# Kernel optimization log

Measured on AMD Instinct MI355X. Metric: run time of the kernel, lower is better.

Reference implementation:

```python
import jax, jax.numpy as jnp
import numpy as np

NEG_INF = -9e15  # matches the torch source's large-negative mask value
LRELU_SLOPE = 0.2


def setup_inputs() -> dict:
    key = jax.random.key(0)
    k1, k2, k3, k4, k5, k6 = jax.random.split(key, 6)
    N, D_IN, D_OUT = 8192, 512, 256
    h = jax.random.normal(k1, (N, D_IN), dtype=jnp.float32)
    adj = jax.random.randint(k2, (N, N), 0, 2, dtype=jnp.int32)
    # xavier_uniform with gain=1.414 for W [out, in] and a [1, 2*out]
    lim_W = 1.414 * np.sqrt(6.0 / (D_IN + D_OUT))
    lim_a = 1.414 * np.sqrt(6.0 / (2 * D_OUT + 1))
    W_w = jax.random.uniform(k3, (D_OUT, D_IN), minval=-lim_W, maxval=lim_W, dtype=jnp.float32)
    W_b = jax.random.normal(k4, (D_OUT,), dtype=jnp.float32) * 0.01
    a_w = jax.random.uniform(k5, (1, 2 * D_OUT), minval=-lim_a, maxval=lim_a, dtype=jnp.float32)
    a_b = jax.random.normal(k6, (1,), dtype=jnp.float32) * 0.01
    return {"h": h, "adj": adj, "W_w": W_w, "W_b": W_b, "a_w": a_w, "a_b": a_b}


def reference(h, adj, W_w, W_b, a_w, a_b):
    # wh = W(h): [N, d_out]
    wh = h @ W_w.T + W_b
    d_out = wh.shape[-1]
    # a(cat([wh_i, wh_j])) decomposes: a_src . wh_i + a_dst . wh_j + a_b
    # (identical math to the O(N^2 * 2d) repeat/cat in the torch source)
    a_src, a_dst = a_w[0, :d_out], a_w[0, d_out:]
    s_src = wh @ a_src  # [N]
    s_dst = wh @ a_dst  # [N]
    e = jax.nn.leaky_relu(s_src[:, None] + s_dst[None, :] + a_b[0], LRELU_SLOPE)  # [N, N]
    masked = jnp.where(adj > 0, e, jnp.float32(NEG_INF))
    attn = jax.nn.softmax(masked, axis=1)  # softmax over neighbors j
    return attn @ wh  # [N, d_out]
```

## Files before the change

kernel.cpp:

```cpp
#include <hip/hip_runtime.h>

typedef unsigned short ushort_t;
typedef unsigned int uint_t;
typedef __attribute__((ext_vector_type(8))) short short8;
typedef __attribute__((ext_vector_type(4))) float f32x4;
typedef __attribute__((ext_vector_type(4))) int i32x4;
typedef __attribute__((ext_vector_type(4))) uint_t u32x4;
typedef __attribute__((ext_vector_type(4))) ushort_t u16x4;

#define LRELU_SLOPE 0.2f

static __device__ __forceinline__ float bf2f(ushort_t h) {
    uint_t u = ((uint_t)h) << 16;
    return __builtin_bit_cast(float, u);
}
static __device__ __forceinline__ ushort_t f2bf(float f) {
    uint_t u = __builtin_bit_cast(uint_t, f);
    uint_t r = (u + 0x7fffu + ((u >> 16) & 1u)) >> 16;
    return (ushort_t)r;
}

static __device__ __forceinline__ void split4(float4 x, uint2& hi, uint2& lo) {
    ushort_t h0 = f2bf(x.x), h1 = f2bf(x.y), h2 = f2bf(x.z), h3 = f2bf(x.w);
    hi.x = (uint_t)h0 | ((uint_t)h1 << 16);
    hi.y = (uint_t)h2 | ((uint_t)h3 << 16);
    float r0 = x.x - bf2f(h0), r1 = x.y - bf2f(h1);
    float r2 = x.z - bf2f(h2), r3 = x.w - bf2f(h3);
    lo.x = (uint_t)f2bf(r0) | ((uint_t)f2bf(r1) << 16);
    lo.y = (uint_t)f2bf(r2) | ((uint_t)f2bf(r3) << 16);
}

__launch_bounds__(256, 2)
__global__ void k1_gemm(const float* __restrict__ h, const float* __restrict__ W,
                        const float* __restrict__ Wb, const float* __restrict__ aw,
                        ushort_t* __restrict__ whT, float* __restrict__ s_src,
                        float* __restrict__ s_dst) {
    __shared__ __align__(16) ushort_t aHi[256 * 40], aLo[256 * 40];
    __shared__ __align__(16) ushort_t bHi[32 * 40], bLo[32 * 40];
    __shared__ float redLds[2][4][32];

    const int t = threadIdx.x;
    const int wv = t >> 6, ln = t & 63;
    const int i0 = blockIdx.x * 32;
    const int srow = t >> 3, sch = t & 7;

    f32x4 acc[4][2];
#pragma unroll
    for (int mt = 0; mt < 4; ++mt)
#pragma unroll
        for (int nt = 0; nt < 2; ++nt) acc[mt][nt] = (f32x4){0.f, 0.f, 0.f, 0.f};

    for (int k0 = 0; k0 < 512; k0 += 32) {
        __syncthreads();
#pragma unroll
        for (int r = 0; r < 8; ++r) {
            float4 x = *(const float4*)(W + (size_t)(r * 32 + srow) * 512 + k0 + sch * 4);
            uint2 hi, lo;
            split4(x, hi, lo);
            *(uint2*)(aHi + (r * 32 + srow) * 40 + sch * 4) = hi;
            *(uint2*)(aLo + (r * 32 + srow) * 40 + sch * 4) = lo;
        }
        {
            float4 x = *(const float4*)(h + (size_t)(i0 + srow) * 512 + k0 + sch * 4);
            uint2 hi, lo;
            split4(x, hi, lo);
            *(uint2*)(bHi + srow * 40 + sch * 4) = hi;
            *(uint2*)(bLo + srow * 40 + sch * 4) = lo;
        }
        __syncthreads();
        {
            short8 bh[2], bl[2];
#pragma unroll
            for (int nt = 0; nt < 2; ++nt) {
                const int boff = (nt * 16 + (ln & 15)) * 40 + (ln >> 4) * 8;
                bh[nt] = *(const short8*)(bHi + boff);
                bl[nt] = *(const short8*)(bLo + boff);
            }
#pragma unroll
            for (int mt = 0; mt < 4; ++mt) {
                const int aoff = (wv * 64 + mt * 16 + (ln & 15)) * 40 + (ln >> 4) * 8;
                short8 ah = *(const short8*)(aHi + aoff);
                short8 al = *(const short8*)(aLo + aoff);
#pragma unroll
                for (int nt = 0; nt < 2; ++nt) {
                    acc[mt][nt] = __builtin_amdgcn_mfma_f32_16x16x32_bf16(ah, bh[nt], acc[mt][nt], 0, 0, 0);
                    acc[mt][nt] = __builtin_amdgcn_mfma_f32_16x16x32_bf16(ah, bl[nt], acc[mt][nt], 0, 0, 0);
                    acc[mt][nt] = __builtin_amdgcn_mfma_f32_16x16x32_bf16(al, bh[nt], acc[mt][nt], 0, 0, 0);
                }
            }
        }
    }

    float psrc[2] = {0.f, 0.f}, pdst[2] = {0.f, 0.f};
#pragma unroll
    for (int mt = 0; mt < 4; ++mt) {
#pragma unroll
        for (int r = 0; r < 4; ++r) {
            const int o = wv * 64 + mt * 16 + (ln >> 4) * 4 + r;
            const float wbv = Wb[o];
            const float as = aw[o];
            const float ad = aw[256 + o];
#pragma unroll
            for (int nt = 0; nt < 2; ++nt) {
                const float v = acc[mt][nt][r] + wbv;
                psrc[nt] += v * as;
                pdst[nt] += v * ad;
                const int i = i0 + nt * 16 + (ln & 15);
                whT[(size_t)o * 8192 + i] = f2bf(v);
            }
        }
    }
#pragma unroll
    for (int off = 16; off < 64; off <<= 1) {
#pragma unroll
        for (int nt = 0; nt < 2; ++nt) {
            psrc[nt] += __shfl_xor(psrc[nt], off, 64);
            pdst[nt] += __shfl_xor(pdst[nt], off, 64);
        }
    }
    if (ln < 16) {
#pragma unroll
        for (int nt = 0; nt < 2; ++nt) {
            redLds[0][wv][nt * 16 + ln] = psrc[nt];
            redLds[1][wv][nt * 16 + ln] = pdst[nt];
        }
    }
    __syncthreads();
    if (t < 32) {
        float s = 0.f;
#pragma unroll
        for (int w = 0; w < 4; ++w) s += redLds[0][w][t];
        s_src[i0 + t] = s;
    } else if (t < 64) {
        float s = 0.f;
#pragma unroll
        for (int w = 0; w < 4; ++w) s += redLds[1][w][t - 32];
        s_dst[i0 + t - 32] = s;
    }
}

__launch_bounds__(512, 2)
__global__ void k2_attn(const int* __restrict__ adj, const ushort_t* __restrict__ whT,
                        const float* __restrict__ s_src, const float* __restrict__ s_dst,
                        const float* __restrict__ ab_p, float* __restrict__ out) {
    __shared__ __align__(16) ushort_t wLds[256 * 72];
    __shared__ __align__(16) ushort_t pLds[32 * 72];
    __shared__ float zLds[32];

    const int t = threadIdx.x;
    const int wv = t >> 6, ln = t & 63;
    const int dq = wv & 3, kh = wv >> 2;
    const int i0 = blockIdx.x * 32;
    const int prow = t >> 4, pjc = t & 15;
    const int srow = t >> 3, sch = t & 7;

    const float ab = ab_p[0];
    const float ssrc = s_src[i0 + prow];

    const int* aBase = adj + (size_t)(i0 + prow) * 8192 + pjc * 4;
    const float* sBase = s_dst + pjc * 4;
    const ushort_t* wBase = whT + (size_t)srow * 8192 + sch * 8;
    ushort_t* pDst = pLds + prow * 72 + pjc * 4;

    f32x4 acc[2][4];
#pragma unroll
    for (int mt = 0; mt < 2; ++mt)
#pragma unroll
        for (int nt = 0; nt < 4; ++nt) acc[mt][nt] = (f32x4){0.f, 0.f, 0.f, 0.f};
    float zacc = 0.f;

    i32x4 Av = *(const i32x4*)aBase;
    f32x4 Sv = *(const f32x4*)sBase;
    u32x4 Wv[4];
#pragma unroll
    for (int r = 0; r < 4; ++r) Wv[r] = *(const u32x4*)(wBase + (size_t)r * 64 * 8192);

    for (int it = 0; it < 128; ++it) {
        const int jn = (it < 127) ? (it + 1) * 64 : it * 64;
        i32x4 Ac = Av;
        f32x4 Sc = Sv;
        u32x4 Wc[4];
#pragma unroll
        for (int r = 0; r < 4; ++r) Wc[r] = Wv[r];
        Av = *(const i32x4*)(aBase + jn);
        Sv = *(const f32x4*)(sBase + jn);
#pragma unroll
        for (int r = 0; r < 4; ++r) Wv[r] = *(const u32x4*)(wBase + (size_t)r * 64 * 8192 + jn);

        __syncthreads();
#pragma unroll
        for (int r = 0; r < 4; ++r)
            *(u32x4*)(wLds + (r * 64 + srow) * 72 + sch * 8) = Wc[r];
        {
            u16x4 pv4;
            float z4 = 0.f;
#pragma unroll
            for (int k = 0; k < 4; ++k) {
                float sc = ssrc + Sc[k] + ab;
                sc = sc > 0.f ? sc : LRELU_SLOPE * sc;
                sc = fminf(sc, 60.f);
                float pv = (Ac[k] > 0) ? __expf(sc) : 0.f;
                z4 += pv;
                pv4[k] = f2bf(pv);
            }
            zacc += z4;
            *(u16x4*)pDst = pv4;
        }
        __syncthreads();
        {
            short8 b[4];
#pragma unroll
            for (int nt = 0; nt < 4; ++nt)
                b[nt] = *(const short8*)(wLds + (dq * 64 + nt * 16 + (ln & 15)) * 72 + kh * 32 + (ln >> 4) * 8);
#pragma unroll
            for (int mt = 0; mt < 2; ++mt) {
                short8 a = *(const short8*)(pLds + (mt * 16 + (ln & 15)) * 72 + kh * 32 + (ln >> 4) * 8);
#pragma unroll
                for (int nt = 0; nt < 4; ++nt)
                    acc[mt][nt] = __builtin_amdgcn_mfma_f32_16x16x32_bf16(a, b[nt], acc[mt][nt], 0, 0, 0);
            }
        }
    }

    zacc += __shfl_xor(zacc, 1, 64);
    zacc += __shfl_xor(zacc, 2, 64);
    zacc += __shfl_xor(zacc, 4, 64);
    zacc += __shfl_xor(zacc, 8, 64);
    if ((t & 15) == 0) zLds[prow] = 1.0f / fmaxf(zacc, 1e-30f);

    __syncthreads();
    float* ex = (float*)wLds;
    if (kh == 1) {
        float* p = ex + (dq * 64 + ln) * 33;
#pragma unroll
        for (int mt = 0; mt < 2; ++mt)
#pragma unroll
            for (int nt = 0; nt < 4; ++nt)
#pragma unroll
                for (int r = 0; r < 4; ++r) p[mt * 16 + nt * 4 + r] = acc[mt][nt][r];
    }
    __syncthreads();
    if (kh == 0) {
        const float* p = ex + (dq * 64 + ln) * 33;
#pragma unroll
        for (int mt = 0; mt < 2; ++mt)
#pragma unroll
            for (int nt = 0; nt < 4; ++nt)
#pragma unroll
                for (int r = 0; r < 4; ++r) {
                    const int il = mt * 16 + (ln >> 4) * 4 + r;
                    const int d = dq * 64 + nt * 16 + (ln & 15);
                    out[(size_t)(i0 + il) * 256 + d] =
                        (acc[mt][nt][r] + p[mt * 16 + nt * 4 + r]) * zLds[il];
                }
    }
}

extern "C" void kernel_launch(void* const* d_in, const int* in_sizes, int n_in, void* d_out,
                              int out_size, void* d_ws, size_t ws_size, hipStream_t stream) {
    int order[16];
    for (int i = 0; i < n_in; ++i) order[i] = i;
    for (int a = 0; a < n_in; ++a)
        for (int b = a + 1; b < n_in; ++b)
            if (in_sizes[order[b]] < in_sizes[order[a]]) {
                int tmp = order[a]; order[a] = order[b]; order[b] = tmp;
            }
    const float* ab = (const float*)d_in[order[0]];
    const float* Wb = (const float*)d_in[order[1]];
    const float* aw = (const float*)d_in[order[2]];
    const float* Ww = (const float*)d_in[order[3]];
    const float* h = (const float*)d_in[order[4]];
    const int* adj = (const int*)d_in[order[5]];

    char* ws = (char*)d_ws;
    ushort_t* whT = (ushort_t*)ws;
    float* ssrc = (float*)(ws + 4194304);
    float* sdst = (float*)(ws + 4194304 + 32768);

    hipLaunchKernelGGL(k1_gemm, dim3(256), dim3(256), 0, stream, h, Ww, Wb, aw, whT, ssrc, sdst);
    hipLaunchKernelGGL(k2_attn, dim3(256), dim3(512), 0, stream, adj, whT, ssrc, sdst, ab,
                       (float*)d_out);
}
```

Baseline: 485.2 us.

## Load MFMA operands directly from global into registers, drop LDS staging and barriers

Each wave now computes its own probability fragments from adj and s_dst and loads whT fragments straight from global memory in MFMA operand layout, so the per-iteration LDS writes, reads and both __syncthreads are removed. This duplicates exp computation and adj/s_dst loads across the four dq waves, and the whT loads become narrower, more scattered accesses. Launch bounds drop to one block per CU to give room for the extra registers, which lowers occupancy.

```diff
diff --git a/kernel.cpp b/kernel.cpp
--- a/kernel.cpp
+++ b/kernel.cpp
@@ -6,7 +6,6 @@
 typedef __attribute__((ext_vector_type(4))) float f32x4;
 typedef __attribute__((ext_vector_type(4))) int i32x4;
 typedef __attribute__((ext_vector_type(4))) uint_t u32x4;
-typedef __attribute__((ext_vector_type(4))) ushort_t u16x4;
 
 #define LRELU_SLOPE 0.2f
 
@@ -139,97 +138,97 @@
     }
 }
 
-__launch_bounds__(512, 2)
+__launch_bounds__(512, 1)
 __global__ void k2_attn(const int* __restrict__ adj, const ushort_t* __restrict__ whT,
                         const float* __restrict__ s_src, const float* __restrict__ s_dst,
                         const float* __restrict__ ab_p, float* __restrict__ out) {
-    __shared__ __align__(16) ushort_t wLds[256 * 72];
-    __shared__ __align__(16) ushort_t pLds[32 * 72];
-    __shared__ float zLds[32];
+    __shared__ float ex[256 * 33];
+    __shared__ float zA[32], zB[32];
 
     const int t = threadIdx.x;
     const int wv = t >> 6, ln = t & 63;
     const int dq = wv & 3, kh = wv >> 2;
     const int i0 = blockIdx.x * 32;
-    const int prow = t >> 4, pjc = t & 15;
-    const int srow = t >> 3, sch = t & 7;
+    const int row0 = ln & 15, kq = ln >> 4;
 
     const float ab = ab_p[0];
-    const float ssrc = s_src[i0 + prow];
-
-    const int* aBase = adj + (size_t)(i0 + prow) * 8192 + pjc * 4;
-    const float* sBase = s_dst + pjc * 4;
-    const ushort_t* wBase = whT + (size_t)srow * 8192 + sch * 8;
-    ushort_t* pDst = pLds + prow * 72 + pjc * 4;
+    const float sb0 = s_src[i0 + row0] + ab;
+    const float sb1 = s_src[i0 + 16 + row0] + ab;
+
+    const int joff = kh * 32 + kq * 8;
+    const int* aBase0 = adj + (size_t)(i0 + row0) * 8192 + joff;
+    const int* aBase1 = adj + (size_t)(i0 + 16 + row0) * 8192 + joff;
+    const float* sBase = s_dst + joff;
+    const ushort_t* wBase = whT + (size_t)(dq * 64 + row0) * 8192 + joff;
 
     f32x4 acc[2][4];
 #pragma unroll
     for (int mt = 0; mt < 2; ++mt)
 #pragma unroll
         for (int nt = 0; nt < 4; ++nt) acc[mt][nt] = (f32x4){0.f, 0.f, 0.f, 0.f};
-    float zacc = 0.f;
-
-    i32x4 Av = *(const i32x4*)aBase;
-    f32x4 Sv = *(const f32x4*)sBase;
-    u32x4 Wv[4];
-#pragma unroll
-    for (int r = 0; r < 4; ++r) Wv[r] = *(const u32x4*)(wBase + (size_t)r * 64 * 8192);
+    float z0 = 0.f, z1 = 0.f;
+
+    i32x4 A0a = *(const i32x4*)aBase0, A0b = *(const i32x4*)(aBase0 + 4);
+    i32x4 A1a = *(const i32x4*)aBase1, A1b = *(const i32x4*)(aBase1 + 4);
+    f32x4 Sa = *(const f32x4*)sBase, Sb = *(const f32x4*)(sBase + 4);
+    short8 Bf[4];
+#pragma unroll
+    for (int nt = 0; nt < 4; ++nt)
+        Bf[nt] = *(const short8*)(wBase + (size_t)nt * 16 * 8192);
 
     for (int it = 0; it < 128; ++it) {
         const int jn = (it < 127) ? (it + 1) * 64 : it * 64;
-        i32x4 Ac = Av;
-        f32x4 Sc = Sv;
-        u32x4 Wc[4];
-#pragma unroll
-        for (int r = 0; r < 4; ++r) Wc[r] = Wv[r];
-        Av = *(const i32x4*)(aBase + jn);
-        Sv = *(const f32x4*)(sBase + jn);
-#pragma unroll
-        for (int r = 0; r < 4; ++r) Wv[r] = *(const u32x4*)(wBase + (size_t)r * 64 * 8192 + jn);
-
-        __syncthreads();
-#pragma unroll
-        for (int r = 0; r < 4; ++r)
-            *(u32x4*)(wLds + (r * 64 + srow) * 72 + sch * 8) = Wc[r];
-        {
-            u16x4 pv4;
-            float z4 = 0.f;
-#pragma unroll
-            for (int k = 0; k < 4; ++k) {
-                float sc = ssrc + Sc[k] + ab;
-                sc = sc > 0.f ? sc : LRELU_SLOPE * sc;
-                sc = fminf(sc, 60.f);
-                float pv = (Ac[k] > 0) ? __expf(sc) : 0.f;
-                z4 += pv;
-                pv4[k] = f2bf(pv);
-            }
-            zacc += z4;
-            *(u16x4*)pDst = pv4;
-        }
-        __syncthreads();
-        {
-            short8 b[4];
-#pragma unroll
-            for (int nt = 0; nt < 4; ++nt)
-                b[nt] = *(const short8*)(wLds + (dq * 64 + nt * 16 + (ln & 15)) * 72 + kh * 32 + (ln >> 4) * 8);
-#pragma unroll
-            for (int mt = 0; mt < 2; ++mt) {
-                short8 a = *(const short8*)(pLds + (mt * 16 + (ln & 15)) * 72 + kh * 32 + (ln >> 4) * 8);
-#pragma unroll
-                for (int nt = 0; nt < 4; ++nt)
-                    acc[mt][nt] = __builtin_amdgcn_mfma_f32_16x16x32_bf16(a, b[nt], acc[mt][nt], 0, 0, 0);
-            }
-        }
-    }
-
-    zacc += __shfl_xor(zacc, 1, 64);
-    zacc += __shfl_xor(zacc, 2, 64);
-    zacc += __shfl_xor(zacc, 4, 64);
-    zacc += __shfl_xor(zacc, 8, 64);
-    if ((t & 15) == 0) zLds[prow] = 1.0f / fmaxf(zacc, 1e-30f);
-
-    __syncthreads();
-    float* ex = (float*)wLds;
+        i32x4 cA0a = A0a, cA0b = A0b, cA1a = A1a, cA1b = A1b;
+        f32x4 cSa = Sa, cSb = Sb;
+        short8 cB[4];
+#pragma unroll
+        for (int nt = 0; nt < 4; ++nt) cB[nt] = Bf[nt];
+        A0a = *(const i32x4*)(aBase0 + jn);
+        A0b = *(const i32x4*)(aBase0 + jn + 4);
+        A1a = *(const i32x4*)(aBase1 + jn);
+        A1b = *(const i32x4*)(aBase1 + jn + 4);
+        Sa = *(const f32x4*)(sBase + jn);
+        Sb = *(const f32x4*)(sBase + jn + 4);
+#pragma unroll
+        for (int nt = 0; nt < 4; ++nt)
+            Bf[nt] = *(const short8*)(wBase + (size_t)nt * 16 * 8192 + jn);
+
+        short8 af0, af1;
+#pragma unroll
+        for (int e = 0; e < 8; ++e) {
+            const float sd = (e < 4) ? cSa[e] : cSb[e - 4];
+            const int a0 = (e < 4) ? cA0a[e] : cA0b[e - 4];
+            const int a1 = (e < 4) ? cA1a[e] : cA1b[e - 4];
+            float t0 = sb0 + sd;
+            float t1 = sb1 + sd;
+            t0 = fminf(fmaxf(t0, LRELU_SLOPE * t0), 60.f);
+            t1 = fminf(fmaxf(t1, LRELU_SLOPE * t1), 60.f);
+            float p0 = (a0 > 0) ? __expf(t0) : 0.f;
+            float p1 = (a1 > 0) ? __expf(t1) : 0.f;
+            z0 += p0;
+            z1 += p1;
+            af0[e] = (short)f2bf(p0);
+            af1[e] = (short)f2bf(p1);
+        }
+#pragma unroll
+        for (int nt = 0; nt < 4; ++nt) {
+            acc[0][nt] = __builtin_amdgcn_mfma_f32_16x16x32_bf16(af0, cB[nt], acc[0][nt], 0, 0, 0);
+            acc[1][nt] = __builtin_amdgcn_mfma_f32_16x16x32_bf16(af1, cB[nt], acc[1][nt], 0, 0, 0);
+        }
+    }
+
+    z0 += __shfl_xor(z0, 16, 64);
+    z0 += __shfl_xor(z0, 32, 64);
+    z1 += __shfl_xor(z1, 16, 64);
+    z1 += __shfl_xor(z1, 32, 64);
+    if (wv == 0 && ln < 16) {
+        zA[row0] = z0;
+        zA[16 + row0] = z1;
+    }
+    if (wv == 4 && ln < 16) {
+        zB[row0] = z0;
+        zB[16 + row0] = z1;
+    }
     if (kh == 1) {
         float* p = ex + (dq * 64 + ln) * 33;
 #pragma unroll
@@ -245,14 +244,16 @@
 #pragma unroll
         for (int mt = 0; mt < 2; ++mt)
 #pragma unroll
-            for (int nt = 0; nt < 4; ++nt)
-#pragma unroll
-                for (int r = 0; r < 4; ++r) {
-                    const int il = mt * 16 + (ln >> 4) * 4 + r;
-                    const int d = dq * 64 + nt * 16 + (ln & 15);
+            for (int r = 0; r < 4; ++r) {
+                const int il = mt * 16 + kq * 4 + r;
+                const float zinv = 1.0f / fmaxf(zA[il] + zB[il], 1e-30f);
+#pragma unroll
+                for (int nt = 0; nt < 4; ++nt) {
+                    const int d = dq * 64 + nt * 16 + row0;
                     out[(size_t)(i0 + il) * 256 + d] =
-                        (acc[mt][nt][r] + p[mt * 16 + nt * 4 + r]) * zLds[il];
+                        (acc[mt][nt][r] + p[mt * 16 + nt * 4 + r]) * zinv;
                 }
+            }
     }
 }
 
```

Result: slower. 609.6 us (+25.6%).

## Split attention over neighbor halves and drop split-bf16 precision in projection GEMM

Applied to the files above, without the earlier changes.

The projection GEMM now casts W and h straight to bf16, replacing the hi/lo split that needed three MFMAs per tile, and uses a 64-wide K step with the LDS laid out to match. The attention kernel can split the neighbor dimension in two, doubling the grid to 512 blocks, which suits a GPU with more CUs than the old 256 blocks could fill. Each half writes partial sums and softmax denominators, and a new normalization kernel combines them. Occupancy hints are raised. In exchange, wh loses precision, and the split path adds an extra kernel launch and an extra read and write of the output-sized buffer.

```diff
diff --git a/kernel.cpp b/kernel.cpp
--- a/kernel.cpp
+++ b/kernel.cpp
@@ -19,15 +19,13 @@
     uint_t r = (u + 0x7fffu + ((u >> 16) & 1u)) >> 16;
     return (ushort_t)r;
 }
-
-static __device__ __forceinline__ void split4(float4 x, uint2& hi, uint2& lo) {
-    ushort_t h0 = f2bf(x.x), h1 = f2bf(x.y), h2 = f2bf(x.z), h3 = f2bf(x.w);
-    hi.x = (uint_t)h0 | ((uint_t)h1 << 16);
-    hi.y = (uint_t)h2 | ((uint_t)h3 << 16);
-    float r0 = x.x - bf2f(h0), r1 = x.y - bf2f(h1);
-    float r2 = x.z - bf2f(h2), r3 = x.w - bf2f(h3);
-    lo.x = (uint_t)f2bf(r0) | ((uint_t)f2bf(r1) << 16);
-    lo.y = (uint_t)f2bf(r2) | ((uint_t)f2bf(r3) << 16);
+static __device__ __forceinline__ uint4 pack8(float4 a, float4 b) {
+    uint4 r;
+    r.x = (uint_t)f2bf(a.x) | ((uint_t)f2bf(a.y) << 16);
+    r.y = (uint_t)f2bf(a.z) | ((uint_t)f2bf(a.w) << 16);
+    r.z = (uint_t)f2bf(b.x) | ((uint_t)f2bf(b.y) << 16);
+    r.w = (uint_t)f2bf(b.z) | ((uint_t)f2bf(b.w) << 16);
+    return r;
 }
 
 __launch_bounds__(256, 2)
@@ -35,14 +33,15 @@
                         const float* __restrict__ Wb, const float* __restrict__ aw,
                         ushort_t* __restrict__ whT, float* __restrict__ s_src,
                         float* __restrict__ s_dst) {
-    __shared__ __align__(16) ushort_t aHi[256 * 40], aLo[256 * 40];
-    __shared__ __align__(16) ushort_t bHi[32 * 40], bLo[32 * 40];
+    __shared__ __align__(16) ushort_t aT[256 * 72];
+    __shared__ __align__(16) ushort_t bT[32 * 72];
     __shared__ float redLds[2][4][32];
 
     const int t = threadIdx.x;
     const int wv = t >> 6, ln = t & 63;
     const int i0 = blockIdx.x * 32;
     const int srow = t >> 3, sch = t & 7;
+    const int row0 = ln & 15, kq = ln >> 4;
 
     f32x4 acc[4][2];
 #pragma unroll
@@ -50,43 +49,34 @@
 #pragma unroll
         for (int nt = 0; nt < 2; ++nt) acc[mt][nt] = (f32x4){0.f, 0.f, 0.f, 0.f};
 
-    for (int k0 = 0; k0 < 512; k0 += 32) {
+    for (int k0 = 0; k0 < 512; k0 += 64) {
         __syncthreads();
 #pragma unroll
         for (int r = 0; r < 8; ++r) {
-            float4 x = *(const float4*)(W + (size_t)(r * 32 + srow) * 512 + k0 + sch * 4);
-            uint2 hi, lo;
-            split4(x, hi, lo);
-            *(uint2*)(aHi + (r * 32 + srow) * 40 + sch * 4) = hi;
-            *(uint2*)(aLo + (r * 32 + srow) * 40 + sch * 4) = lo;
+            const float* gp = W + (size_t)(r * 32 + srow) * 512 + k0 + sch * 8;
+            float4 x0 = *(const float4*)gp;
+            float4 x1 = *(const float4*)(gp + 4);
+            *(uint4*)(aT + (r * 32 + srow) * 72 + sch * 8) = pack8(x0, x1);
         }
         {
-            float4 x = *(const float4*)(h + (size_t)(i0 + srow) * 512 + k0 + sch * 4);
-            uint2 hi, lo;
-            split4(x, hi, lo);
-            *(uint2*)(bHi + srow * 40 + sch * 4) = hi;
-            *(uint2*)(bLo + srow * 40 + sch * 4) = lo;
+            const float* gp = h + (size_t)(i0 + srow) * 512 + k0 + sch * 8;
+            float4 x0 = *(const float4*)gp;
+            float4 x1 = *(const float4*)(gp + 4);
+            *(uint4*)(bT + srow * 72 + sch * 8) = pack8(x0, x1);
         }
         __syncthreads();
-        {
-            short8 bh[2], bl[2];
-#pragma unroll
-            for (int nt = 0; nt < 2; ++nt) {
-                const int boff = (nt * 16 + (ln & 15)) * 40 + (ln >> 4) * 8;
-                bh[nt] = *(const short8*)(bHi + boff);
-                bl[nt] = *(const short8*)(bLo + boff);
-            }
+#pragma unroll
+        for (int ks = 0; ks < 2; ++ks) {
+            short8 b[2];
+#pragma unroll
+            for (int nt = 0; nt < 2; ++nt)
+                b[nt] = *(const short8*)(bT + (nt * 16 + row0) * 72 + ks * 32 + kq * 8);
 #pragma unroll
             for (int mt = 0; mt < 4; ++mt) {
-                const int aoff = (wv * 64 + mt * 16 + (ln & 15)) * 40 + (ln >> 4) * 8;
-                short8 ah = *(const short8*)(aHi + aoff);
-                short8 al = *(const short8*)(aLo + aoff);
-#pragma unroll
-                for (int nt = 0; nt < 2; ++nt) {
-                    acc[mt][nt] = __builtin_amdgcn_mfma_f32_16x16x32_bf16(ah, bh[nt], acc[mt][nt], 0, 0, 0);
-                    acc[mt][nt] = __builtin_amdgcn_mfma_f32_16x16x32_bf16(ah, bl[nt], acc[mt][nt], 0, 0, 0);
-                    acc[mt][nt] = __builtin_amdgcn_mfma_f32_16x16x32_bf16(al, bh[nt], acc[mt][nt], 0, 0, 0);
-                }
+                short8 a = *(const short8*)(aT + (wv * 64 + mt * 16 + row0) * 72 + ks * 32 + kq * 8);
+#pragma unroll
+                for (int nt = 0; nt < 2; ++nt)
+                    acc[mt][nt] = __builtin_amdgcn_mfma_f32_16x16x32_bf16(a, b[nt], acc[mt][nt], 0, 0, 0);
             }
         }
     }
@@ -139,10 +129,11 @@
     }
 }
 
-__launch_bounds__(512, 2)
+__launch_bounds__(512, 4)
 __global__ void k2_attn(const int* __restrict__ adj, const ushort_t* __restrict__ whT,
                         const float* __restrict__ s_src, const float* __restrict__ s_dst,
-                        const float* __restrict__ ab_p, float* __restrict__ out) {
+                        const float* __restrict__ ab_p, float* __restrict__ out0,
+                        float* __restrict__ out1, float* __restrict__ zp, int jsplit) {
     __shared__ __align__(16) ushort_t wLds[256 * 72];
     __shared__ __align__(16) ushort_t pLds[32 * 72];
     __shared__ float zLds[32];
@@ -150,16 +141,22 @@
     const int t = threadIdx.x;
     const int wv = t >> 6, ln = t & 63;
     const int dq = wv & 3, kh = wv >> 2;
-    const int i0 = blockIdx.x * 32;
+    const int split2 = (jsplit == 2);
+    const int jb = split2 ? (int)(blockIdx.x & 1) : 0;
+    const int ib = split2 ? (int)(blockIdx.x >> 1) : (int)blockIdx.x;
+    const int i0 = ib * 32;
+    const int jlen = split2 ? 4096 : 8192;
+    const int jbase = jb * jlen;
+    const int iters = jlen >> 6;
     const int prow = t >> 4, pjc = t & 15;
     const int srow = t >> 3, sch = t & 7;
 
     const float ab = ab_p[0];
     const float ssrc = s_src[i0 + prow];
 
-    const int* aBase = adj + (size_t)(i0 + prow) * 8192 + pjc * 4;
-    const float* sBase = s_dst + pjc * 4;
-    const ushort_t* wBase = whT + (size_t)srow * 8192 + sch * 8;
+    const int* aBase = adj + (size_t)(i0 + prow) * 8192 + jbase + pjc * 4;
+    const float* sBase = s_dst + jbase + pjc * 4;
+    const ushort_t* wBase = whT + (size_t)srow * 8192 + jbase + sch * 8;
     ushort_t* pDst = pLds + prow * 72 + pjc * 4;
 
     f32x4 acc[2][4];
@@ -175,8 +172,8 @@
 #pragma unroll
     for (int r = 0; r < 4; ++r) Wv[r] = *(const u32x4*)(wBase + (size_t)r * 64 * 8192);
 
-    for (int it = 0; it < 128; ++it) {
-        const int jn = (it < 127) ? (it + 1) * 64 : it * 64;
+    for (int it = 0; it < iters; ++it) {
+        const int jn = (it < iters - 1) ? (it + 1) * 64 : it * 64;
         i32x4 Ac = Av;
         f32x4 Sc = Sv;
         u32x4 Wc[4];
@@ -226,7 +223,11 @@
     zacc += __shfl_xor(zacc, 2, 64);
     zacc += __shfl_xor(zacc, 4, 64);
     zacc += __shfl_xor(zacc, 8, 64);
-    if ((t & 15) == 0) zLds[prow] = 1.0f / fmaxf(zacc, 1e-30f);
+    if (split2) {
+        if ((t & 15) == 0) zp[(size_t)jb * 8192 + i0 + prow] = zacc;
+    } else {
+        if ((t & 15) == 0) zLds[prow] = 1.0f / fmaxf(zacc, 1e-30f);
+    }
 
     __syncthreads();
     float* ex = (float*)wLds;
@@ -241,6 +242,7 @@
     }
     __syncthreads();
     if (kh == 0) {
+        float* outp = (jb == 0) ? out0 : out1;
         const float* p = ex + (dq * 64 + ln) * 33;
 #pragma unroll
         for (int mt = 0; mt < 2; ++mt)
@@ -250,10 +252,21 @@
                 for (int r = 0; r < 4; ++r) {
                     const int il = mt * 16 + (ln >> 4) * 4 + r;
                     const int d = dq * 64 + nt * 16 + (ln & 15);
-                    out[(size_t)(i0 + il) * 256 + d] =
-                        (acc[mt][nt][r] + p[mt * 16 + nt * 4 + r]) * zLds[il];
+                    const float v = acc[mt][nt][r] + p[mt * 16 + nt * 4 + r];
+                    if (split2)
+                        outp[(size_t)(i0 + il) * 256 + d] = v;
+                    else
+                        outp[(size_t)(i0 + il) * 256 + d] = v * zLds[il];
                 }
     }
+}
+
+__global__ void k3_norm(float* __restrict__ out, const float* __restrict__ part,
+                        const float* __restrict__ zp) {
+    const int i = blockIdx.x, t = threadIdx.x;
+    const float rz = 1.0f / fmaxf(zp[i] + zp[8192 + i], 1e-30f);
+    const size_t idx = (size_t)i * 256 + t;
+    out[idx] = (out[idx] + part[idx]) * rz;
 }
 
 extern "C" void kernel_launch(void* const* d_in, const int* in_sizes, int n_in, void* d_out,
@@ -275,9 +288,15 @@
     char* ws = (char*)d_ws;
     ushort_t* whT = (ushort_t*)ws;
     float* ssrc = (float*)(ws + 4194304);
-    float* sdst = (float*)(ws + 4194304 + 32768);
+    float* sdst = (float*)(ws + 4227072);
+    float* part = (float*)(ws + 4259840);
+    float* zp = (float*)(ws + 12648448);
+    const size_t need = 12713984;
+    const int jsplit = (ws_size >= need) ? 2 : 1;
 
     hipLaunchKernelGGL(k1_gemm, dim3(256), dim3(256), 0, stream, h, Ww, Wb, aw, whT, ssrc, sdst);
-    hipLaunchKernelGGL(k2_attn, dim3(256), dim3(512), 0, stream, adj, whT, ssrc, sdst, ab,
-                       (float*)d_out);
-}
+    hipLaunchKernelGGL(k2_attn, dim3(256 * jsplit), dim3(512), 0, stream, adj, whT, ssrc, sdst,
+                       ab, (float*)d_out, part, zp, jsplit);
+    if (jsplit == 2)
+        hipLaunchKernelGGL(k3_norm, dim3(8192), dim3(256), 0, stream, (float*)d_out, part, zp);
+}
```

Result: faster. 443.6 us (-8.6%).
